# Kernel optimization log

Hardware: AMD Instinct MI355X
Metric: run time of the kernel (lower is better)

The kernel has to match this reference:

```python
import jax, jax.numpy as jnp
import numpy as np

T, B, OBS, D, H = 512, 256, 256, 512, 512  # time, batch, obs_dim, embed/gru hidden, critic hidden


def setup_inputs() -> dict:
    key = jax.random.key(0)
    ks = jax.random.split(key, 10)
    s = lambda fan_in: 1.0 / np.sqrt(fan_in)
    return {
        "obs": jax.random.normal(ks[0], (T, B, OBS), dtype=jnp.float32),
        "done": jax.random.bernoulli(ks[1], 0.01, (T, B)),
        "hstate": jnp.zeros((B, D), dtype=jnp.float32),
        # embedding dense
        "W_emb": jax.random.normal(ks[2], (OBS, D), dtype=jnp.float32) * s(OBS),
        "b_emb": jnp.zeros((D,), dtype=jnp.float32),
        # GRU: input kernels [D, 3D] (r|z|n), hidden kernels [D, 3D], input bias [3D], hn bias [D]
        "Wi": jax.random.normal(ks[3], (D, 3 * D), dtype=jnp.float32) * s(D),
        "bi": jnp.zeros((3 * D,), dtype=jnp.float32),
        "Wh": jax.random.normal(ks[4], (D, 3 * D), dtype=jnp.float32) * s(D),
        "bhn": jnp.zeros((D,), dtype=jnp.float32),
        # critic MLP
        "W1": jax.random.normal(ks[5], (D, H), dtype=jnp.float32) * s(D),
        "b1": jnp.zeros((H,), dtype=jnp.float32),
        "W2": jax.random.normal(ks[6], (H, 1), dtype=jnp.float32) * s(H),
        "b2": jnp.zeros((1,), dtype=jnp.float32),
    }


def _forward(obs, done, hstate, W_emb, b_emb, Wi, bi, Wh, bhn, W1, b1, W2, b2):
    # embedding: [T, B, D]
    emb = jax.nn.relu(jnp.einsum("tbo,od->tbd", obs, W_emb) + b_emb)
    # precompute input-side gate preactivations for all timesteps: [T, B, 3D]
    xg = jnp.einsum("tbd,de->tbe", emb, Wi) + bi

    def step(h, inp):
        xg_t, d_t = inp
        # reset carry where episode ended (flax GRU init carry is zeros)
        h = jnp.where(d_t[:, None], 0.0, h)
        hg = h @ Wh  # [B, 3D]
        r = jax.nn.sigmoid(xg_t[:, :D] + hg[:, :D])
        z = jax.nn.sigmoid(xg_t[:, D:2 * D] + hg[:, D:2 * D])
        n = jnp.tanh(xg_t[:, 2 * D:] + r * (hg[:, 2 * D:] + bhn))
        h_new = (1.0 - z) * n + z * h
        return h_new, h_new

    h_last, ys = jax.lax.scan(step, hstate, (xg, done))  # ys: [T, B, D]
    critic = jax.nn.relu(jnp.einsum("tbd,dh->tbh", ys, W1) + b1)
    value = jnp.squeeze(jnp.einsum("tbh,ho->tbo", critic, W2) + b2, axis=-1)  # [T, B]
    return h_last, value


def reference(obs, done, hstate, W_emb, b_emb, Wi, bi, Wh, bhn, W1, b1, W2, b2):
    return _forward(obs, done, hstate, W_emb, b_emb, Wi, bi, Wh, bhn, W1, b1, W2, b2)
```

## Files before the change

kernel.cpp:

```cpp
#include <hip/hip_runtime.h>

#define TT   512
#define BB   256
#define OBSD 256
#define DD   512
#define HH   512
#define MROWS (TT*BB)

typedef __attribute__((ext_vector_type(8))) short short8;
typedef __attribute__((ext_vector_type(4))) float f32x4;

__device__ __forceinline__ ushort f2b(float f){
  unsigned int x = __float_as_uint(f);
  x = (x + 0x7fffu + ((x >> 16) & 1u)) >> 16;
  return (ushort)x;
}
__device__ __forceinline__ float b2f(ushort u){
  return __uint_as_float(((unsigned int)u) << 16);
}
__device__ __forceinline__ float sigm(float x){ return 1.f/(1.f + __expf(-x)); }
__device__ __forceinline__ float tanh_f(float x){ return 1.f - 2.f/(__expf(2.f*x) + 1.f); }

__global__ void k_transpose_bf16(const float* __restrict__ W, ushort* __restrict__ Wt,
                                 int K, int N){
  int i = blockIdx.x*256 + threadIdx.x;
  if(i >= K*N) return;
  int k = i / N, n = i % N;
  Wt[(size_t)n*K + k] = f2b(W[i]);
}

__global__ void k_f32_to_bf16(const float* __restrict__ in, ushort* __restrict__ out,
                              int n4){
  int i = blockIdx.x*256 + threadIdx.x;
  if(i >= n4) return;
  const float4 v = ((const float4*)in)[i];
  union{ ushort u[4]; uint2 d; } p;
  p.u[0] = f2b(v.x); p.u[1] = f2b(v.y); p.u[2] = f2b(v.z); p.u[3] = f2b(v.w);
  ((uint2*)out)[i] = p.d;
}

__global__ void k_detect(const int* __restrict__ done, int* __restrict__ flag){
  __shared__ int cnt;
  if(threadIdx.x == 0) cnt = 0;
  __syncthreads();
  int c = 0;
  for(int i = threadIdx.x; i < 32768; i += 256) c += (done[i] != 0);
  for(int off = 32; off; off >>= 1) c += __shfl_down(c, off, 64);
  if((threadIdx.x & 63) == 0) atomicAdd(&cnt, c);
  __syncthreads();
  if(threadIdx.x == 0) *flag = (cnt > 700) ? 1 : 0;
}

#define GSTAGE(buf, k0v) { \
  _Pragma("unroll") \
  for(int j = 0; j < 2; j++){ \
    const int flat = tid*16 + j*4096;         \
    const int rw  = flat >> 6;                \
    const int ke  = (flat & 63) >> 1;         \
    __builtin_amdgcn_global_load_lds( \
      (const __attribute__((address_space(1))) void*)(A + (m0+rw)*(size_t)K + (k0v) + ke), \
      (__attribute__((address_space(3))) void*)((char*)As[buf] + flat), 16, 0, 0); \
    __builtin_amdgcn_global_load_lds( \
      (const __attribute__((address_space(1))) void*)(Bt + (n0+rw)*(size_t)K + (k0v) + ke), \
      (__attribute__((address_space(3))) void*)((char*)Bs[buf] + flat), 16, 0, 0); \
  } }
#define GCOMPUTE(buf) { \
    short8 af[4], bf[4]; \
    _Pragma("unroll") for(int mi=0;mi<4;mi++) \
      af[mi] = *(const short8*)((const char*)As[buf] + (wr*64+mi*16+l16)*64 + l4*16); \
    _Pragma("unroll") for(int ni=0;ni<4;ni++) \
      bf[ni] = *(const short8*)((const char*)Bs[buf] + (wc*64+ni*16+l16)*64 + l4*16); \
    _Pragma("unroll") for(int mi=0;mi<4;mi++) \
      _Pragma("unroll") for(int ni=0;ni<4;ni++) \
        acc[mi][ni] = __builtin_amdgcn_mfma_f32_16x16x32_bf16(af[mi], bf[ni], acc[mi][ni], 0,0,0); }

__global__ __launch_bounds__(256) void k_gemm128(const ushort* __restrict__ A,
                                                 const ushort* __restrict__ Bt,
                                                 const float* __restrict__ bias,
                                                 ushort* __restrict__ C,
                                                 int M, int N, int K, int relu,
                                                 int xg_layout,
                                                 float* __restrict__ vpart,
                                                 const float* __restrict__ W2f){
  __shared__ __align__(16) ushort As[2][4096];
  __shared__ __align__(16) ushort Bs[2][4096];
  const int tid = threadIdx.x;
  const int l = tid & 63, l16 = l & 15, l4 = l >> 4;
  const int w = tid >> 6, wr = w >> 1, wc = w & 1;
  const size_t m0 = (size_t)blockIdx.x*128, n0 = (size_t)blockIdx.y*128;
  f32x4 acc[4][4] = {};

  GSTAGE(0, 0);
  asm volatile("s_waitcnt vmcnt(0)" ::: "memory");
  __syncthreads();
  int cur = 0;
  for(int k0 = 32; k0 < K; k0 += 32){
    GSTAGE(cur^1, k0);
    GCOMPUTE(cur);
    asm volatile("s_waitcnt vmcnt(0)" ::: "memory");
    __syncthreads();
    cur ^= 1;
  }
  GCOMPUTE(cur);

  if(vpart){
    float w2v[4];
    float bv[4];
    #pragma unroll
    for(int ni=0;ni<4;ni++){
      const int col = (int)n0 + wc*64 + ni*16 + l16;
      w2v[ni] = W2f[col];
      bv[ni]  = bias[col];
    }
    #pragma unroll
    for(int mi=0;mi<4;mi++){
      #pragma unroll
      for(int r=0;r<4;r++){
        float s = 0.f;
        #pragma unroll
        for(int ni=0;ni<4;ni++){
          float v = acc[mi][ni][r] + bv[ni];
          v = fmaxf(v, 0.f);
          s += v * w2v[ni];
        }
        #pragma unroll
        for(int off=1; off<16; off<<=1) s += __shfl_xor(s, off, 16);
        if(l16 == 0){
          const int row = (int)m0 + wr*64 + mi*16 + l4*4 + r;
          vpart[(size_t)(blockIdx.y*2 + wc)*M + row] = s;
        }
      }
    }
    return;
  }

  #pragma unroll
  for(int ni=0;ni<4;ni++){
    const int col = (int)n0 + wc*64 + ni*16 + l16;
    const float bv = bias[col];
    #pragma unroll
    for(int mi=0;mi<4;mi++){
      #pragma unroll
      for(int r=0;r<4;r++){
        const int row = (int)m0 + wr*64 + mi*16 + l4*4 + r;
        float v = acc[mi][ni][r] + bv;
        if(relu) v = fmaxf(v, 0.f);
        size_t addr;
        if(xg_layout){
          const int tl = row >> 8, brow = row & 255;
          const int gg = brow >> 5, r32 = brow & 31;
          const int gate = col >> 9, cw = col & 511, ds2 = cw >> 4, c16 = cw & 15;
          addr = ((((size_t)tl*32 + ds2)*8 + gg)*3 + gate)*512 + r32*16 + c16;
        } else {
          addr = (size_t)row*N + col;
        }
        C[addr] = f2b(v);
      }
    }
  }
}

__global__ __launch_bounds__(256) void k_value_reduce(const float* __restrict__ vp,
                                                      const float* __restrict__ b2,
                                                      float* __restrict__ val, int M){
  int i = blockIdx.x*256 + threadIdx.x;
  if(i >= M) return;
  float s = b2[0];
  #pragma unroll
  for(int cb=0; cb<8; cb++) s += vp[(size_t)cb*M + i];
  val[i] = s;
}

__device__ __forceinline__ void bar_slow(int* cntA, int g, int ds, int target, int tid){
  asm volatile("s_waitcnt vmcnt(0)" ::: "memory");
  __syncthreads();
  if(tid == 0)
    __hip_atomic_store(cntA + g*32 + ds, target,
                       __ATOMIC_RELAXED, __HIP_MEMORY_SCOPE_AGENT);
  if(tid < 32){
    const int* fp = cntA + g*32 + tid;
    while(__hip_atomic_load(fp, __ATOMIC_RELAXED, __HIP_MEMORY_SCOPE_AGENT) < target)
      __builtin_amdgcn_s_sleep(1);
  }
  __syncthreads();
}

__device__ __forceinline__ void bar_fast(int* cntL, int* cntA, int g, int ds,
                                         int target, int tid){
  asm volatile("s_waitcnt vmcnt(0)" ::: "memory");
  __syncthreads();
  if(tid == 0){
    int* pL = cntL + g*32 + ds;
    asm volatile("global_atomic_swap %0, %1, off" :: "v"(pL), "v"(target) : "memory");
    __hip_atomic_store(cntA + g*32 + ds, target,
                       __ATOMIC_RELAXED, __HIP_MEMORY_SCOPE_AGENT);
  }
  if(tid < 32){
    int* fpL = cntL + g*32 + tid;
    const int* fpA = cntA + g*32 + tid;
    int it = 0;
    for(;;){
      int old;
      asm volatile("global_atomic_add %0, %1, %2, off sc0"
                   : "=v"(old) : "v"(fpL), "v"(0) : "memory");
      asm volatile("s_waitcnt vmcnt(0)" ::: "memory");
      if(old >= target) break;
      if((++it & 15) == 0 &&
         __hip_atomic_load(fpA, __ATOMIC_RELAXED, __HIP_MEMORY_SCOPE_AGENT) >= target)
        break;
      __builtin_amdgcn_s_sleep(1);
    }
  }
  __syncthreads();
  asm volatile("buffer_inv sc0" ::: "memory");
}

#define ALD_S(v, j) { const ushort* pj_ = hgrp + (j)*1024; \
  asm volatile("global_load_dwordx4 %0, %1, off sc0 sc1" : "=&v"(v) : "v"(pj_)); }
#define ALD_F(v, j) { const ushort* pj_ = hgrp + (j)*1024; \
  asm volatile("global_load_dwordx4 %0, %1, off" : "=&v"(v) : "v"(pj_)); }
#define DECL_A short8 a0,a1,a2,a3,a4,a5,a6,a7,a8,a9,a10,a11,a12,a13,a14,a15
#define ALOADS(M) M(a0,0);M(a1,1);M(a2,2);M(a3,3);M(a4,4);M(a5,5);M(a6,6);M(a7,7); \
  M(a8,8);M(a9,9);M(a10,10);M(a11,11);M(a12,12);M(a13,13);M(a14,14);M(a15,15)
#define ZERO_A { const short8 z = {0,0,0,0,0,0,0,0}; \
  a0=z;a1=z;a2=z;a3=z;a4=z;a5=z;a6=z;a7=z;a8=z;a9=z;a10=z;a11=z;a12=z;a13=z;a14=z;a15=z; }
#define STEPK(ak, k0lit) { const int kboff = ((k0lit + l4*8) << 1); \
  _Pragma("unroll") for(int gi=0; gi<3; gi++){ \
    const short8 wf = *(const short8*)((const char*)whs + ((rb[gi] + kboff) ^ sw[gi])); \
    acc[gi] = __builtin_amdgcn_mfma_f32_16x16x32_bf16(wf, ak, acc[gi], 0, 0, 0); } }
#define MFMA48 STEPK(a0,0) STEPK(a1,32) STEPK(a2,64) STEPK(a3,96) STEPK(a4,128) \
  STEPK(a5,160) STEPK(a6,192) STEPK(a7,224) STEPK(a8,256) STEPK(a9,288) STEPK(a10,320) \
  STEPK(a11,352) STEPK(a12,384) STEPK(a13,416) STEPK(a14,448) STEPK(a15,480)
#define XG_PREFETCH(tls, nb) { \
  const ushort* slb_ = xg + (((size_t)(tls)*32 + ds)*8 + g)*1536; \
  const int q0_ = m ? 512 : 0; \
  __builtin_amdgcn_global_load_lds( \
    (const __attribute__((address_space(1))) void*)(slb_ + q0_ + l*8), \
    (__attribute__((address_space(3))) void*)(&xgs[nb][q0_]), 16, 0, 0); \
  __builtin_amdgcn_global_load_lds( \
    (const __attribute__((address_space(1))) void*)(slb_ + 1024 + l*8), \
    (__attribute__((address_space(3))) void*)(&xgs[nb][1024]), 16, 0, 0); }
#define GRU_EPI(pv) { \
  const uint2 xru = *(const uint2*)&xgs[cur][        r32*16 + l4*4]; \
  const uint2 xzu = *(const uint2*)&xgs[cur][ 512 +  r32*16 + l4*4]; \
  const uint2 xnu = *(const uint2*)&xgs[cur][1024 +  r32*16 + l4*4]; \
  const ushort xr4[4] = {(ushort)(xru.x&0xffff),(ushort)(xru.x>>16), \
                         (ushort)(xru.y&0xffff),(ushort)(xru.y>>16)}; \
  const ushort xz4[4] = {(ushort)(xzu.x&0xffff),(ushort)(xzu.x>>16), \
                         (ushort)(xzu.y&0xffff),(ushort)(xzu.y>>16)}; \
  const ushort xn4[4] = {(ushort)(xnu.x&0xffff),(ushort)(xnu.x>>16), \
                         (ushort)(xnu.y&0xffff),(ushort)(xnu.y>>16)}; \
  const float bhv[4] = {bh4.x, bh4.y, bh4.z, bh4.w}; \
  union{ ushort u[4]; uint2 v; } p; \
  _Pragma("unroll") for(int r=0;r<4;r++){ \
    const float hold = dn ? 0.f : hf[r]; \
    const float rg = sigm(b2f(xr4[r]) + acc[0][r]); \
    const float zg = sigm(b2f(xz4[r]) + acc[1][r]); \
    const float ng = tanh_f(b2f(xn4[r]) + rg*(acc[2][r] + bhv[r])); \
    const float hv = (1.f - zg)*ng + zg*hold; \
    hf[r] = hv; p.u[r] = f2b(hv); } \
  pv = p.v; }

__global__ __launch_bounds__(128, 1) void k_scan_coop(
    const ushort* __restrict__ xg,
    const void* __restrict__ donep,
    const int* __restrict__ flagp, const float* __restrict__ h_in,
    const ushort* __restrict__ WhT, const float* __restrict__ bhn,
    ushort* __restrict__ ys, float* __restrict__ h_io,
    float* __restrict__ h_last, ushort* __restrict__ hbf,
    int t0, int steps, int* __restrict__ cntbase, int* __restrict__ xcc_tab){
  __shared__ __align__(16) ushort whs[48*512];
  __shared__ __align__(16) ushort xgs[2][1536];
  __shared__ unsigned char dns[512*32];
  __shared__ int fastf;
  const int tid = threadIdx.x;
  const int m = tid >> 6, l = tid & 63, l16 = l & 15, l4 = l >> 4;
  const int bid = blockIdx.x;
  const int g = bid & 7, ds = bid >> 3;
  const int use8 = *flagp;
  const unsigned char* d8 = (const unsigned char*)donep;
  const int* d32 = (const int*)donep;
  int* cntL = cntbase;
  int* cntA = cntbase + 256;

  for(int e = tid; e < 3072; e += 128){
    const int lr = e >> 6;
    const int kc = (e & 63) << 3;
    const int grow_w = (lr >> 4)*DD + ds*16 + (lr & 15);
    short8 v = *(const short8*)(WhT + (size_t)grow_w*DD + kc);
    int boff = ((lr << 10) + (kc << 1)) ^ ((lr & 7) << 4);
    *(short8*)((char*)whs + boff) = v;
  }
  for(int e = tid; e < steps*32; e += 128){
    const int tloc = e >> 5, r = e & 31;
    const int gi = (t0 + tloc)*BB + g*32 + r;
    dns[e] = use8 ? (d8[gi] != 0) : (d32[gi] != 0);
  }

  const int r32 = m*16 + l16;
  const int row = g*32 + r32;
  const int d0  = ds*16 + l4*4;
  const float4 bh4 = *(const float4*)(bhn + d0);

  float hf[4];
  {
    const float4 hv4 = *(const float4*)(h_in + (size_t)row*DD + d0);
    hf[0]=hv4.x; hf[1]=hv4.y; hf[2]=hv4.z; hf[3]=hv4.w;
    union{ ushort u[4]; uint2 v; } p;
    #pragma unroll
    for(int r=0;r<4;r++) p.u[r] = f2b(hf[r]);
    const ushort* pp = hbf + (size_t)g*16384 + ds*512 + r32*16 + l4*4;
    asm volatile("global_store_dwordx2 %0, %1, off sc0 sc1" :: "v"(pp), "v"(p.v) : "memory");
  }
  XG_PREFETCH(0, 0);
  int my_xcc;
  asm volatile("s_getreg_b32 %0, hwreg(HW_REG_XCC_ID)" : "=s"(my_xcc));
  if(tid == 0){
    int* p = xcc_tab + bid;
    asm volatile("global_store_dword %0, %1, off sc0 sc1" :: "v"(p), "v"(my_xcc) : "memory");
  }
  bar_slow(cntA, g, ds, 1, tid);
  {
    int bad = 0;
    if(tid < 32){
      const int* p = xcc_tab + tid*8 + g;
      int v;
      asm volatile("global_load_dword %0, %1, off sc0 sc1" : "=v"(v) : "v"(p) : "memory");
      asm volatile("s_waitcnt vmcnt(0)" ::: "memory");
      bad = (v != my_xcc);
    }
    const int anybad = __any(bad);
    if(tid == 0) fastf = !anybad;
    __syncthreads();
  }
  const int fast = fastf;

  int rb[3], sw[3];
  #pragma unroll
  for(int gi=0; gi<3; gi++){
    const int lr = gi*16 + l16;
    rb[gi] = lr << 10;
    sw[gi] = (lr & 7) << 4;
  }
  const ushort* hb0 = hbf;
  const ushort* hb1 = hbf + (size_t)BB*DD;
  const size_t csub = (size_t)((l4>>1) << 9) + (size_t)r32*16 + ((l4&1) << 3);
  int cur = 0;

  if(fast){
    asm volatile("buffer_inv sc0" ::: "memory");
    for(int tl = 0; tl < steps; tl++){
      const ushort* hcur = (tl & 1) ? hb1 : hb0;
      ushort* hnxt = (ushort*)((tl & 1) ? hb0 : hb1);
      const bool dn = dns[tl*32 + r32];
      const ushort* hgrp = hcur + (size_t)g*16384 + csub;
      DECL_A;
      ALOADS(ALD_F);
      __builtin_amdgcn_sched_barrier(0);
      if(tl + 1 < steps){
        XG_PREFETCH(tl+1, cur^1);
        __builtin_amdgcn_sched_barrier(0);
        asm volatile("s_waitcnt vmcnt(2)" ::: "memory");
      } else {
        asm volatile("s_waitcnt vmcnt(0)" ::: "memory");
      }
      __builtin_amdgcn_sched_barrier(0);
      if(__builtin_expect(dn, 0)) ZERO_A;
      f32x4 acc[3] = {};
      MFMA48;
      uint2 pv;
      GRU_EPI(pv);
      const ushort* pp = hnxt + (size_t)g*16384 + ds*512 + r32*16 + l4*4;
      asm volatile("global_store_dwordx2 %0, %1, off" :: "v"(pp), "v"(pv) : "memory");
      bar_fast(cntL, cntA, g, ds, tl + 2, tid);
      *(uint2*)(ys + ((size_t)tl*BB + row)*DD + d0) = pv;
      cur ^= 1;
    }
  } else {
    for(int tl = 0; tl < steps; tl++){
      const ushort* hcur = (tl & 1) ? hb1 : hb0;
      ushort* hnxt = (ushort*)((tl & 1) ? hb0 : hb1);
      const bool dn = dns[tl*32 + r32];
      const ushort* hgrp = hcur + (size_t)g*16384 + csub;
      DECL_A;
      ALOADS(ALD_S);
      __builtin_amdgcn_sched_barrier(0);
      if(tl + 1 < steps){
        XG_PREFETCH(tl+1, cur^1);
        __builtin_amdgcn_sched_barrier(0);
        asm volatile("s_waitcnt vmcnt(2)" ::: "memory");
      } else {
        asm volatile("s_waitcnt vmcnt(0)" ::: "memory");
      }
      __builtin_amdgcn_sched_barrier(0);
      if(__builtin_expect(dn, 0)) ZERO_A;
      f32x4 acc[3] = {};
      MFMA48;
      uint2 pv;
      GRU_EPI(pv);
      const ushort* pp = hnxt + (size_t)g*16384 + ds*512 + r32*16 + l4*4;
      asm volatile("global_store_dwordx2 %0, %1, off sc0 sc1" :: "v"(pp), "v"(pv) : "memory");
      bar_slow(cntA, g, ds, tl + 2, tid);
      *(uint2*)(ys + ((size_t)tl*BB + row)*DD + d0) = pv;
      cur ^= 1;
    }
  }

  {
    float4 o; o.x=hf[0]; o.y=hf[1]; o.z=hf[2]; o.w=hf[3];
    *(float4*)(h_io   + (size_t)row*DD + d0) = o;
    *(float4*)(h_last + (size_t)row*DD + d0) = o;
  }
}

__global__ __launch_bounds__(1024) void k_scan(const ushort* __restrict__ xg,
                                               const void* __restrict__ donep,
                                               const int* __restrict__ flagp,
                                               const float* __restrict__ h_in,
                                               const ushort* __restrict__ WhT,
                                               const float* __restrict__ bhn,
                                               ushort* __restrict__ ys,
                                               float* __restrict__ h_io,
                                               float* __restrict__ h_last,
                                               int t0, int steps){
  __shared__ __align__(16) float  h_f[16][DD];
  __shared__ __align__(16) ushort h_b[16][DD];
  const int tid = threadIdx.x;
  const int w = tid >> 6, l = tid & 63, l16 = l & 15, l4 = l >> 4;
  const int b0 = blockIdx.x * 16;
  const int use8 = *flagp;
  const unsigned char* d8 = (const unsigned char*)donep;
  const int* d32 = (const int*)donep;

  for(int e = tid; e < 16*DD; e += 1024){
    int b = e >> 9, dd = e & (DD-1);
    float v = h_in[(size_t)(b0 + b)*DD + dd];
    h_f[b][dd] = v; h_b[b][dd] = f2b(v);
  }
  __syncthreads();

  const int dbase = w * 32;
  const ushort* bp[6];
  #pragma unroll
  for(int g=0; g<3; g++)
    #pragma unroll
    for(int nt=0; nt<2; nt++)
      bp[g*2+nt] = WhT + (size_t)(g*DD + dbase + nt*16 + l16) * DD;

  for(int tl = 0; tl < steps; tl++){
    const int drow = (t0 + tl)*BB + b0;
    const bool dnA = use8 ? (d8[drow + l16] != 0) : (d32[drow + l16] != 0);
    f32x4 acc[3][2] = {};
    const short8 zf = {0,0,0,0,0,0,0,0};
    for(int k0 = 0; k0 < DD; k0 += 32){
      const int kb = k0 + l4*8;
      short8 a = *(const short8*)&h_b[l16][kb];
      if(dnA) a = zf;
      #pragma unroll
      for(int g=0; g<3; g++)
        #pragma unroll
        for(int nt=0; nt<2; nt++){
          const short8 b = *(const short8*)(bp[g*2+nt] + kb);
          acc[g][nt] = __builtin_amdgcn_mfma_f32_16x16x32_bf16(a, b, acc[g][nt], 0, 0, 0);
        }
    }
    float hnew[2][4];
    #pragma unroll
    for(int nt=0; nt<2; nt++){
      const int dd = dbase + nt*16 + l16;
      const float bh = bhn[dd];
      const int ds2 = dd >> 4, c16 = dd & 15;
      #pragma unroll
      for(int r=0; r<4; r++){
        const int brow = l4*4 + r;
        const int grow = b0 + brow;
        const int gg = grow >> 5, r32 = grow & 31;
        const bool dn = use8 ? (d8[drow + brow] != 0) : (d32[drow + brow] != 0);
        const size_t sbase = (((size_t)tl*32 + ds2)*8 + gg)*1536 + r32*16 + c16;
        const float xr = b2f(xg[sbase]);
        const float xz = b2f(xg[sbase + 512]);
        const float xn = b2f(xg[sbase + 1024]);
        const float hold = dn ? 0.f : h_f[brow][dd];
        const float rg = sigm(xr + acc[0][nt][r]);
        const float zg = sigm(xz + acc[1][nt][r]);
        const float ng = tanh_f(xn + rg*(acc[2][nt][r] + bh));
        hnew[nt][r] = (1.f - zg)*ng + zg*hold;
      }
    }
    __syncthreads();
    #pragma unroll
    for(int nt=0; nt<2; nt++){
      const int dd = dbase + nt*16 + l16;
      #pragma unroll
      for(int r=0; r<4; r++){
        const int brow = l4*4 + r;
        const size_t rowl = (size_t)(tl*BB + b0 + brow);
        const float hv = hnew[nt][r];
        h_f[brow][dd] = hv;
        h_b[brow][dd] = f2b(hv);
        ys[rowl*DD + dd] = f2b(hv);
      }
    }
    __syncthreads();
  }

  for(int e = tid; e < 16*DD; e += 1024){
    int b = e >> 9, dd = e & (DD-1);
    float v = h_f[b][dd];
    h_io[(size_t)(b0 + b)*DD + dd] = v;
    h_last[(size_t)(b0 + b)*DD + dd] = v;
  }
}

extern "C" void kernel_launch(void* const* d_in, const int* in_sizes, int n_in,
                              void* d_out, int out_size, void* d_ws, size_t ws_size,
                              hipStream_t stream){
  const float* obs    = (const float*)d_in[0];
  const void*  done   = d_in[1];
  const float* hstate = (const float*)d_in[2];
  const float* W_emb  = (const float*)d_in[3];
  const float* b_emb  = (const float*)d_in[4];
  const float* Wi     = (const float*)d_in[5];
  const float* bi     = (const float*)d_in[6];
  const float* Wh     = (const float*)d_in[7];
  const float* bhn    = (const float*)d_in[8];
  const float* W1     = (const float*)d_in[9];
  const float* b1     = (const float*)d_in[10];
  const float* W2     = (const float*)d_in[11];
  const float* b2     = (const float*)d_in[12];
  float* out = (float*)d_out;
  char*  ws  = (char*)d_ws;

  ushort* WembT = (ushort*)(ws + 0);
  ushort* WiT   = (ushort*)(ws + 262144);
  ushort* WhT   = (ushort*)(ws + 1835008);
  ushort* W1T   = (ushort*)(ws + 3407872);
  int*    flag  = (int*)   (ws + 3932160);
  float*  hio   = (float*) (ws + 3936256);
  ushort* hbf   = (ushort*)(ws + 4460544);
  int*    cnt   = (int*)   (ws + 4984832);
  int*    xcc   = (int*)   (ws + 5017600);
  const size_t FIX = 5242880;

  int TC = 0;
  {
    const int cands[6] = {512, 256, 128, 64, 32, 16};
    for(int i = 0; i < 6; i++){
      size_t need = FIX + (size_t)cands[i] * 1310720u;
      if(need <= ws_size){ TC = cands[i]; break; }
    }
  }
  if(TC == 0) return;

  ushort* emb_c  = (ushort*)(ws + FIX);
  ushort* xg_c   = (ushort*)(ws + FIX + (size_t)TC*262144u);
  ushort* ys_c   = (ushort*)(ws + FIX + (size_t)TC*1048576u);
  float*  vpart  = (float*)emb_c;
  ushort* obs_bf = ys_c;

  k_transpose_bf16<<<(OBSD*DD+255)/256, 256, 0, stream>>>(W_emb, WembT, OBSD, DD);
  k_transpose_bf16<<<(DD*3*DD+255)/256, 256, 0, stream>>>(Wi, WiT, DD, 3*DD);
  k_transpose_bf16<<<(DD*3*DD+255)/256, 256, 0, stream>>>(Wh, WhT, DD, 3*DD);
  k_transpose_bf16<<<(DD*HH+255)/256, 256, 0, stream>>>(W1, W1T, DD, HH);
  k_detect<<<1, 256, 0, stream>>>((const int*)done, flag);

  const int nchunks = TT / TC;
  for(int c = 0; c < nchunks; c++){
    const int Mc = TC * BB;
    const size_t row0 = (size_t)c * Mc;
    k_f32_to_bf16<<<(Mc*OBSD/4 + 255)/256, 256, 0, stream>>>(obs + row0*OBSD, obs_bf,
                                                             Mc*OBSD/4);
    k_gemm128<<<dim3(Mc/128, DD/128), 256, 0, stream>>>(obs_bf, WembT, b_emb,
                                                        emb_c, Mc, DD, OBSD, 1, 0,
                                                        nullptr, nullptr);
    k_gemm128<<<dim3(Mc/128, (3*DD)/128), 256, 0, stream>>>(emb_c, WiT, bi,
                                                            xg_c, Mc, 3*DD, DD, 0, 1,
                                                            nullptr, nullptr);
    {
      const ushort* xg_a = xg_c;  const void* done_a = done;
      const int* flag_a = flag;   const float* hin_a = (c == 0) ? hstate : hio;
      const ushort* wht_a = WhT;  const float* bhn_a = bhn;
      ushort* ys_a = ys_c;        float* hio_a = hio;
      float* hl_a = out;          ushort* hbf_a = hbf;
      int t0_a = c*TC;            int steps_a = TC;
      int* cnt_a = cnt;           int* xcc_a = xcc;
      void* args[14] = { (void*)&xg_a, (void*)&done_a, (void*)&flag_a, (void*)&hin_a,
                         (void*)&wht_a, (void*)&bhn_a, (void*)&ys_a, (void*)&hio_a,
                         (void*)&hl_a, (void*)&hbf_a, (void*)&t0_a, (void*)&steps_a,
                         (void*)&cnt_a, (void*)&xcc_a };
      hipMemsetAsync(cnt, 0, 4096, stream);
      hipError_t err = hipLaunchCooperativeKernel((const void*)k_scan_coop,
                                                  dim3(256), dim3(128), args, 0, stream);
      if(err != hipSuccess){
        k_scan<<<16, 1024, 0, stream>>>(xg_c, done, flag, hin_a, WhT, bhn,
                                        ys_c, hio, out, c*TC, TC);
      }
    }
    k_gemm128<<<dim3(Mc/128, HH/128), 256, 0, stream>>>(ys_c, W1T, b1,
                                                        nullptr, Mc, HH, DD, 1, 0,
                                                        vpart, W2);
    k_value_reduce<<<(Mc + 255)/256, 256, 0, stream>>>(vpart, b2,
                                                       out + (size_t)BB*DD + row0, Mc);
  }
}
```

Baseline: 2.783 ms.

## Fuse critic MLP into cooperative GRU scan using per-step hidden loads

The critic first layer and its W2 reduction now run inside the scan kernel. Each block keeps a 16-column slice of W1 in shared memory and reuses the hidden-state fragments it already loads for step t to compute the critic output for step t-1. Per-block partial values go to a 32-way partial buffer, which a reduce kernel sums. This drops the ys write and the separate critic GEMM pass, but adds 16 MFMAs plus shuffles to every serial scan step and another 16 KB of LDS. The non-cooperative fallback keeps the old path.

```diff
diff --git a/kernel.cpp b/kernel.cpp
--- a/kernel.cpp
+++ b/kernel.cpp
@@ -104,8 +104,7 @@
   GCOMPUTE(cur);
 
   if(vpart){
-    float w2v[4];
-    float bv[4];
+    float w2v[4], bv[4];
     #pragma unroll
     for(int ni=0;ni<4;ni++){
       const int col = (int)n0 + wc*64 + ni*16 + l16;
@@ -162,12 +161,12 @@
 
 __global__ __launch_bounds__(256) void k_value_reduce(const float* __restrict__ vp,
                                                       const float* __restrict__ b2,
-                                                      float* __restrict__ val, int M){
+                                                      float* __restrict__ val, int M,
+                                                      int nparts){
   int i = blockIdx.x*256 + threadIdx.x;
   if(i >= M) return;
   float s = b2[0];
-  #pragma unroll
-  for(int cb=0; cb<8; cb++) s += vp[(size_t)cb*M + i];
+  for(int cb = 0; cb < nparts; cb++) s += vp[(size_t)cb*M + i];
   val[i] = s;
 }
 
@@ -231,6 +230,21 @@
 #define MFMA48 STEPK(a0,0) STEPK(a1,32) STEPK(a2,64) STEPK(a3,96) STEPK(a4,128) \
   STEPK(a5,160) STEPK(a6,192) STEPK(a7,224) STEPK(a8,256) STEPK(a9,288) STEPK(a10,320) \
   STEPK(a11,352) STEPK(a12,384) STEPK(a13,416) STEPK(a14,448) STEPK(a15,480)
+#define CSTEP(ak, k0lit) { const int kboff = ((k0lit + l4*8) << 1); \
+  const short8 wf = *(const short8*)((const char*)w1s + ((rbc + kboff) ^ swc)); \
+  accc = __builtin_amdgcn_mfma_f32_16x16x32_bf16(wf, ak, accc, 0, 0, 0); }
+#define CRITIC16 CSTEP(a0,0) CSTEP(a1,32) CSTEP(a2,64) CSTEP(a3,96) CSTEP(a4,128) \
+  CSTEP(a5,160) CSTEP(a6,192) CSTEP(a7,224) CSTEP(a8,256) CSTEP(a9,288) CSTEP(a10,320) \
+  CSTEP(a11,352) CSTEP(a12,384) CSTEP(a13,416) CSTEP(a14,448) CSTEP(a15,480)
+#define CRITIC_EPI(tcr) { \
+  float s = 0.f; \
+  _Pragma("unroll") for(int r=0;r<4;r++){ \
+    float v = accc[r] + b1v[r]; \
+    v = fmaxf(v, 0.f); \
+    s += v * w2v[r]; } \
+  s += __shfl_xor(s, 16, 64); \
+  s += __shfl_xor(s, 32, 64); \
+  if(l4 == 0) vpart[(size_t)ds*Mc + (size_t)(tcr)*BB + row] = s; }
 #define XG_PREFETCH(tls, nb) { \
   const ushort* slb_ = xg + (((size_t)(tls)*32 + ds)*8 + g)*1536; \
   const int q0_ = m ? 512 : 0; \
@@ -265,11 +279,15 @@
     const ushort* __restrict__ xg,
     const void* __restrict__ donep,
     const int* __restrict__ flagp, const float* __restrict__ h_in,
-    const ushort* __restrict__ WhT, const float* __restrict__ bhn,
-    ushort* __restrict__ ys, float* __restrict__ h_io,
-    float* __restrict__ h_last, ushort* __restrict__ hbf,
+    const ushort* __restrict__ WhT, const ushort* __restrict__ W1T,
+    const float* __restrict__ bhn, const float* __restrict__ b1,
+    const float* __restrict__ W2f,
+    float* __restrict__ h_io, float* __restrict__ h_last,
+    ushort* __restrict__ hbf,
+    float* __restrict__ vpart,
     int t0, int steps, int* __restrict__ cntbase, int* __restrict__ xcc_tab){
   __shared__ __align__(16) ushort whs[48*512];
+  __shared__ __align__(16) ushort w1s[16*512];
   __shared__ __align__(16) ushort xgs[2][1536];
   __shared__ unsigned char dns[512*32];
   __shared__ int fastf;
@@ -282,6 +300,7 @@
   const int* d32 = (const int*)donep;
   int* cntL = cntbase;
   int* cntA = cntbase + 256;
+  const int Mc = steps*BB;
 
   for(int e = tid; e < 3072; e += 128){
     const int lr = e >> 6;
@@ -291,6 +310,13 @@
     int boff = ((lr << 10) + (kc << 1)) ^ ((lr & 7) << 4);
     *(short8*)((char*)whs + boff) = v;
   }
+  for(int e = tid; e < 1024; e += 128){
+    const int lr = e >> 6;
+    const int kc = (e & 63) << 3;
+    short8 v = *(const short8*)(W1T + (size_t)(ds*16 + lr)*DD + kc);
+    int boff = ((lr << 10) + (kc << 1)) ^ ((lr & 7) << 4);
+    *(short8*)((char*)w1s + boff) = v;
+  }
   for(int e = tid; e < steps*32; e += 128){
     const int tloc = e >> 5, r = e & 31;
     const int gi = (t0 + tloc)*BB + g*32 + r;
@@ -301,6 +327,14 @@
   const int row = g*32 + r32;
   const int d0  = ds*16 + l4*4;
   const float4 bh4 = *(const float4*)(bhn + d0);
+  float b1v[4], w2v[4];
+  {
+    const float4 b1f = *(const float4*)(b1 + d0);
+    const float4 w2f = *(const float4*)(W2f + d0);
+    b1v[0]=b1f.x; b1v[1]=b1f.y; b1v[2]=b1f.z; b1v[3]=b1f.w;
+    w2v[0]=w2f.x; w2v[1]=w2f.y; w2v[2]=w2f.z; w2v[3]=w2f.w;
+  }
+  const int rbc = l16 << 10, swc = (l16 & 7) << 4;
 
   float hf[4];
   {
@@ -365,6 +399,11 @@
         asm volatile("s_waitcnt vmcnt(0)" ::: "memory");
       }
       __builtin_amdgcn_sched_barrier(0);
+      f32x4 accc = {};
+      if(tl > 0){
+        CRITIC16;
+        CRITIC_EPI(tl-1);
+      }
       if(__builtin_expect(dn, 0)) ZERO_A;
       f32x4 acc[3] = {};
       MFMA48;
@@ -373,8 +412,18 @@
       const ushort* pp = hnxt + (size_t)g*16384 + ds*512 + r32*16 + l4*4;
       asm volatile("global_store_dwordx2 %0, %1, off" :: "v"(pp), "v"(pv) : "memory");
       bar_fast(cntL, cntA, g, ds, tl + 2, tid);
-      *(uint2*)(ys + ((size_t)tl*BB + row)*DD + d0) = pv;
       cur ^= 1;
+    }
+    {
+      const ushort* hfin = (steps & 1) ? hb1 : hb0;
+      const ushort* hgrp = hfin + (size_t)g*16384 + csub;
+      DECL_A;
+      ALOADS(ALD_F);
+      asm volatile("s_waitcnt vmcnt(0)" ::: "memory");
+      __builtin_amdgcn_sched_barrier(0);
+      f32x4 accc = {};
+      CRITIC16;
+      CRITIC_EPI(steps-1);
     }
   } else {
     for(int tl = 0; tl < steps; tl++){
@@ -393,6 +442,11 @@
         asm volatile("s_waitcnt vmcnt(0)" ::: "memory");
       }
       __builtin_amdgcn_sched_barrier(0);
+      f32x4 accc = {};
+      if(tl > 0){
+        CRITIC16;
+        CRITIC_EPI(tl-1);
+      }
       if(__builtin_expect(dn, 0)) ZERO_A;
       f32x4 acc[3] = {};
       MFMA48;
@@ -401,8 +455,18 @@
       const ushort* pp = hnxt + (size_t)g*16384 + ds*512 + r32*16 + l4*4;
       asm volatile("global_store_dwordx2 %0, %1, off sc0 sc1" :: "v"(pp), "v"(pv) : "memory");
       bar_slow(cntA, g, ds, tl + 2, tid);
-      *(uint2*)(ys + ((size_t)tl*BB + row)*DD + d0) = pv;
       cur ^= 1;
+    }
+    {
+      const ushort* hfin = (steps & 1) ? hb1 : hb0;
+      const ushort* hgrp = hfin + (size_t)g*16384 + csub;
+      DECL_A;
+      ALOADS(ALD_S);
+      asm volatile("s_waitcnt vmcnt(0)" ::: "memory");
+      __builtin_amdgcn_sched_barrier(0);
+      f32x4 accc = {};
+      CRITIC16;
+      CRITIC_EPI(steps-1);
     }
   }
 
@@ -576,30 +640,40 @@
     k_gemm128<<<dim3(Mc/128, (3*DD)/128), 256, 0, stream>>>(emb_c, WiT, bi,
                                                             xg_c, Mc, 3*DD, DD, 0, 1,
                                                             nullptr, nullptr);
+    hipError_t err;
     {
       const ushort* xg_a = xg_c;  const void* done_a = done;
       const int* flag_a = flag;   const float* hin_a = (c == 0) ? hstate : hio;
-      const ushort* wht_a = WhT;  const float* bhn_a = bhn;
-      ushort* ys_a = ys_c;        float* hio_a = hio;
-      float* hl_a = out;          ushort* hbf_a = hbf;
+      const ushort* wht_a = WhT;  const ushort* w1t_a = W1T;
+      const float* bhn_a = bhn;   const float* b1_a = b1;
+      const float* w2_a = W2;
+      float* hio_a = hio;         float* hl_a = out;
+      ushort* hbf_a = hbf;        float* vp_a = vpart;
       int t0_a = c*TC;            int steps_a = TC;
       int* cnt_a = cnt;           int* xcc_a = xcc;
-      void* args[14] = { (void*)&xg_a, (void*)&done_a, (void*)&flag_a, (void*)&hin_a,
-                         (void*)&wht_a, (void*)&bhn_a, (void*)&ys_a, (void*)&hio_a,
-                         (void*)&hl_a, (void*)&hbf_a, (void*)&t0_a, (void*)&steps_a,
+      void* args[17] = { (void*)&xg_a, (void*)&done_a, (void*)&flag_a, (void*)&hin_a,
+                         (void*)&wht_a, (void*)&w1t_a, (void*)&bhn_a, (void*)&b1_a,
+                         (void*)&w2_a, (void*)&hio_a, (void*)&hl_a, (void*)&hbf_a,
+                         (void*)&vp_a, (void*)&t0_a, (void*)&steps_a,
                          (void*)&cnt_a, (void*)&xcc_a };
       hipMemsetAsync(cnt, 0, 4096, stream);
-      hipError_t err = hipLaunchCooperativeKernel((const void*)k_scan_coop,
-                                                  dim3(256), dim3(128), args, 0, stream);
-      if(err != hipSuccess){
-        k_scan<<<16, 1024, 0, stream>>>(xg_c, done, flag, hin_a, WhT, bhn,
-                                        ys_c, hio, out, c*TC, TC);
-      }
-    }
-    k_gemm128<<<dim3(Mc/128, HH/128), 256, 0, stream>>>(ys_c, W1T, b1,
-                                                        nullptr, Mc, HH, DD, 1, 0,
-                                                        vpart, W2);
-    k_value_reduce<<<(Mc + 255)/256, 256, 0, stream>>>(vpart, b2,
-                                                       out + (size_t)BB*DD + row0, Mc);
-  }
-}
+      err = hipLaunchCooperativeKernel((const void*)k_scan_coop,
+                                       dim3(256), dim3(128), args, 0, stream);
+    }
+    if(err == hipSuccess){
+      k_value_reduce<<<(Mc + 255)/256, 256, 0, stream>>>(vpart, b2,
+                                                         out + (size_t)BB*DD + row0,
+                                                         Mc, 32);
+    } else {
+      const float* hin_a = (c == 0) ? hstate : hio;
+      k_scan<<<16, 1024, 0, stream>>>(xg_c, done, flag, hin_a, WhT, bhn,
+                                      ys_c, hio, out, c*TC, TC);
+      k_gemm128<<<dim3(Mc/128, HH/128), 256, 0, stream>>>(ys_c, W1T, b1,
+                                                          nullptr, Mc, HH, DD, 1, 0,
+                                                          vpart, W2);
+      k_value_reduce<<<(Mc + 255)/256, 256, 0, stream>>>(vpart, b2,
+                                                         out + (size_t)BB*DD + row0,
+                                                         Mc, 8);
+    }
+  }
+}
```

After: 2.883 ms. 3.6% more time.

## Split GRU scan into 512 single-wave blocks over 16-row batch groups

Applied to the files above, without the earlier changes.

The cooperative GRU scan moves from 256 blocks of two waves (32 batch rows per group) to 512 blocks of one wave (16 rows per group). The xg layout, hidden-state buffer layout, done-flag staging, barrier counter offsets and xcc table indexing are all rewritten for 16-row groups. The aim is to shrink intra-block synchronisation and spread the recurrence across more independent blocks. The cost is that each block still stages the full Wh slice into LDS, so weight-loading traffic and LDS use per CU double, and more blocks take part in the cross-block barriers.

```diff
diff --git a/kernel.cpp b/kernel.cpp
--- a/kernel.cpp
+++ b/kernel.cpp
@@ -104,8 +104,7 @@
   GCOMPUTE(cur);
 
   if(vpart){
-    float w2v[4];
-    float bv[4];
+    float w2v[4], bv[4];
     #pragma unroll
     for(int ni=0;ni<4;ni++){
       const int col = (int)n0 + wc*64 + ni*16 + l16;
@@ -148,9 +147,9 @@
         size_t addr;
         if(xg_layout){
           const int tl = row >> 8, brow = row & 255;
-          const int gg = brow >> 5, r32 = brow & 31;
+          const int gg = brow >> 4, r16 = brow & 15;
           const int gate = col >> 9, cw = col & 511, ds2 = cw >> 4, c16 = cw & 15;
-          addr = ((((size_t)tl*32 + ds2)*8 + gg)*3 + gate)*512 + r32*16 + c16;
+          addr = ((((size_t)tl*32 + ds2)*16 + gg)*3 + gate)*256 + r16*16 + c16;
         } else {
           addr = (size_t)row*N + col;
         }
@@ -162,12 +161,12 @@
 
 __global__ __launch_bounds__(256) void k_value_reduce(const float* __restrict__ vp,
                                                       const float* __restrict__ b2,
-                                                      float* __restrict__ val, int M){
+                                                      float* __restrict__ val, int M,
+                                                      int nparts){
   int i = blockIdx.x*256 + threadIdx.x;
   if(i >= M) return;
   float s = b2[0];
-  #pragma unroll
-  for(int cb=0; cb<8; cb++) s += vp[(size_t)cb*M + i];
+  for(int cb = 0; cb < nparts; cb++) s += vp[(size_t)cb*M + i];
   val[i] = s;
 }
 
@@ -215,9 +214,9 @@
   asm volatile("buffer_inv sc0" ::: "memory");
 }
 
-#define ALD_S(v, j) { const ushort* pj_ = hgrp + (j)*1024; \
+#define ALD_S(v, j) { const ushort* pj_ = hgrp + (j)*512; \
   asm volatile("global_load_dwordx4 %0, %1, off sc0 sc1" : "=&v"(v) : "v"(pj_)); }
-#define ALD_F(v, j) { const ushort* pj_ = hgrp + (j)*1024; \
+#define ALD_F(v, j) { const ushort* pj_ = hgrp + (j)*512; \
   asm volatile("global_load_dwordx4 %0, %1, off" : "=&v"(v) : "v"(pj_)); }
 #define DECL_A short8 a0,a1,a2,a3,a4,a5,a6,a7,a8,a9,a10,a11,a12,a13,a14,a15
 #define ALOADS(M) M(a0,0);M(a1,1);M(a2,2);M(a3,3);M(a4,4);M(a5,5);M(a6,6);M(a7,7); \
@@ -232,18 +231,18 @@
   STEPK(a5,160) STEPK(a6,192) STEPK(a7,224) STEPK(a8,256) STEPK(a9,288) STEPK(a10,320) \
   STEPK(a11,352) STEPK(a12,384) STEPK(a13,416) STEPK(a14,448) STEPK(a15,480)
 #define XG_PREFETCH(tls, nb) { \
-  const ushort* slb_ = xg + (((size_t)(tls)*32 + ds)*8 + g)*1536; \
-  const int q0_ = m ? 512 : 0; \
+  const ushort* slb_ = xg + (((size_t)(tls)*32 + ds)*16 + g)*768; \
   __builtin_amdgcn_global_load_lds( \
-    (const __attribute__((address_space(1))) void*)(slb_ + q0_ + l*8), \
-    (__attribute__((address_space(3))) void*)(&xgs[nb][q0_]), 16, 0, 0); \
+    (const __attribute__((address_space(1))) void*)(slb_ + l*8), \
+    (__attribute__((address_space(3))) void*)(&xgs[nb][0]), 16, 0, 0); \
   __builtin_amdgcn_global_load_lds( \
-    (const __attribute__((address_space(1))) void*)(slb_ + 1024 + l*8), \
-    (__attribute__((address_space(3))) void*)(&xgs[nb][1024]), 16, 0, 0); }
+    (const __attribute__((address_space(1))) void*)(slb_ + 256 + l*8), \
+    (__attribute__((address_space(3))) void*)(&xgs[nb][256]), 16, 0, 0); }
 #define GRU_EPI(pv) { \
-  const uint2 xru = *(const uint2*)&xgs[cur][        r32*16 + l4*4]; \
-  const uint2 xzu = *(const uint2*)&xgs[cur][ 512 +  r32*16 + l4*4]; \
-  const uint2 xnu = *(const uint2*)&xgs[cur][1024 +  r32*16 + l4*4]; \
+  const int xb = l16*16 + l4*4; \
+  const uint2 xru = *(const uint2*)&xgs[cur][      xb]; \
+  const uint2 xzu = *(const uint2*)&xgs[cur][256 + xb]; \
+  const uint2 xnu = *(const uint2*)&xgs[cur][512 + xb]; \
   const ushort xr4[4] = {(ushort)(xru.x&0xffff),(ushort)(xru.x>>16), \
                          (ushort)(xru.y&0xffff),(ushort)(xru.y>>16)}; \
   const ushort xz4[4] = {(ushort)(xzu.x&0xffff),(ushort)(xzu.x>>16), \
@@ -261,7 +260,7 @@
     hf[r] = hv; p.u[r] = f2b(hv); } \
   pv = p.v; }
 
-__global__ __launch_bounds__(128, 1) void k_scan_coop(
+__global__ __launch_bounds__(64, 1) void k_scan_coop(
     const ushort* __restrict__ xg,
     const void* __restrict__ donep,
     const int* __restrict__ flagp, const float* __restrict__ h_in,
@@ -270,20 +269,21 @@
     float* __restrict__ h_last, ushort* __restrict__ hbf,
     int t0, int steps, int* __restrict__ cntbase, int* __restrict__ xcc_tab){
   __shared__ __align__(16) ushort whs[48*512];
-  __shared__ __align__(16) ushort xgs[2][1536];
-  __shared__ unsigned char dns[512*32];
+  __shared__ __align__(16) ushort xgs[2][768];
+  __shared__ unsigned char dns[512*16];
   __shared__ int fastf;
   const int tid = threadIdx.x;
-  const int m = tid >> 6, l = tid & 63, l16 = l & 15, l4 = l >> 4;
+  const int l = tid, l16 = l & 15, l4 = l >> 4;
   const int bid = blockIdx.x;
-  const int g = bid & 7, ds = bid >> 3;
+  const int g = ((bid & 7) << 1) | ((bid >> 3) & 1);
+  const int ds = bid >> 4;
   const int use8 = *flagp;
   const unsigned char* d8 = (const unsigned char*)donep;
   const int* d32 = (const int*)donep;
   int* cntL = cntbase;
-  int* cntA = cntbase + 256;
-
-  for(int e = tid; e < 3072; e += 128){
+  int* cntA = cntbase + 512;
+
+  for(int e = tid; e < 3072; e += 64){
     const int lr = e >> 6;
     const int kc = (e & 63) << 3;
     const int grow_w = (lr >> 4)*DD + ds*16 + (lr & 15);
@@ -291,14 +291,13 @@
     int boff = ((lr << 10) + (kc << 1)) ^ ((lr & 7) << 4);
     *(short8*)((char*)whs + boff) = v;
   }
-  for(int e = tid; e < steps*32; e += 128){
-    const int tloc = e >> 5, r = e & 31;
-    const int gi = (t0 + tloc)*BB + g*32 + r;
+  for(int e = tid; e < steps*16; e += 64){
+    const int tloc = e >> 4, r = e & 15;
+    const int gi = (t0 + tloc)*BB + g*16 + r;
     dns[e] = use8 ? (d8[gi] != 0) : (d32[gi] != 0);
   }
 
-  const int r32 = m*16 + l16;
-  const int row = g*32 + r32;
+  const int row = g*16 + l16;
   const int d0  = ds*16 + l4*4;
   const float4 bh4 = *(const float4*)(bhn + d0);
 
@@ -309,7 +308,7 @@
     union{ ushort u[4]; uint2 v; } p;
     #pragma unroll
     for(int r=0;r<4;r++) p.u[r] = f2b(hf[r]);
-    const ushort* pp = hbf + (size_t)g*16384 + ds*512 + r32*16 + l4*4;
+    const ushort* pp = hbf + (size_t)g*8192 + ds*256 + l16*16 + l4*4;
     asm volatile("global_store_dwordx2 %0, %1, off sc0 sc1" :: "v"(pp), "v"(p.v) : "memory");
   }
   XG_PREFETCH(0, 0);
@@ -323,7 +322,7 @@
   {
     int bad = 0;
     if(tid < 32){
-      const int* p = xcc_tab + tid*8 + g;
+      const int* p = xcc_tab + tid*16 + (g & 1)*8 + (g >> 1);
       int v;
       asm volatile("global_load_dword %0, %1, off sc0 sc1" : "=v"(v) : "v"(p) : "memory");
       asm volatile("s_waitcnt vmcnt(0)" ::: "memory");
@@ -344,7 +343,7 @@
   }
   const ushort* hb0 = hbf;
   const ushort* hb1 = hbf + (size_t)BB*DD;
-  const size_t csub = (size_t)((l4>>1) << 9) + (size_t)r32*16 + ((l4&1) << 3);
+  const size_t csub = (size_t)((l4>>1) << 8) + (size_t)l16*16 + ((l4&1) << 3);
   int cur = 0;
 
   if(fast){
@@ -352,8 +351,8 @@
     for(int tl = 0; tl < steps; tl++){
       const ushort* hcur = (tl & 1) ? hb1 : hb0;
       ushort* hnxt = (ushort*)((tl & 1) ? hb0 : hb1);
-      const bool dn = dns[tl*32 + r32];
-      const ushort* hgrp = hcur + (size_t)g*16384 + csub;
+      const bool dn = dns[tl*16 + l16];
+      const ushort* hgrp = hcur + (size_t)g*8192 + csub;
       DECL_A;
       ALOADS(ALD_F);
       __builtin_amdgcn_sched_barrier(0);
@@ -370,7 +369,7 @@
       MFMA48;
       uint2 pv;
       GRU_EPI(pv);
-      const ushort* pp = hnxt + (size_t)g*16384 + ds*512 + r32*16 + l4*4;
+      const ushort* pp = hnxt + (size_t)g*8192 + ds*256 + l16*16 + l4*4;
       asm volatile("global_store_dwordx2 %0, %1, off" :: "v"(pp), "v"(pv) : "memory");
       bar_fast(cntL, cntA, g, ds, tl + 2, tid);
       *(uint2*)(ys + ((size_t)tl*BB + row)*DD + d0) = pv;
@@ -380,8 +379,8 @@
     for(int tl = 0; tl < steps; tl++){
       const ushort* hcur = (tl & 1) ? hb1 : hb0;
       ushort* hnxt = (ushort*)((tl & 1) ? hb0 : hb1);
-      const bool dn = dns[tl*32 + r32];
-      const ushort* hgrp = hcur + (size_t)g*16384 + csub;
+      const bool dn = dns[tl*16 + l16];
+      const ushort* hgrp = hcur + (size_t)g*8192 + csub;
       DECL_A;
       ALOADS(ALD_S);
       __builtin_amdgcn_sched_barrier(0);
@@ -398,7 +397,7 @@
       MFMA48;
       uint2 pv;
       GRU_EPI(pv);
-      const ushort* pp = hnxt + (size_t)g*16384 + ds*512 + r32*16 + l4*4;
+      const ushort* pp = hnxt + (size_t)g*8192 + ds*256 + l16*16 + l4*4;
       asm volatile("global_store_dwordx2 %0, %1, off sc0 sc1" :: "v"(pp), "v"(pv) : "memory");
       bar_slow(cntA, g, ds, tl + 2, tid);
       *(uint2*)(ys + ((size_t)tl*BB + row)*DD + d0) = pv;
@@ -474,12 +473,12 @@
       for(int r=0; r<4; r++){
         const int brow = l4*4 + r;
         const int grow = b0 + brow;
-        const int gg = grow >> 5, r32 = grow & 31;
+        const int gg = grow >> 4, r16 = grow & 15;
         const bool dn = use8 ? (d8[drow + brow] != 0) : (d32[drow + brow] != 0);
-        const size_t sbase = (((size_t)tl*32 + ds2)*8 + gg)*1536 + r32*16 + c16;
+        const size_t sbase = ((((size_t)tl*32 + ds2)*16 + gg)*3)*256 + r16*16 + c16;
         const float xr = b2f(xg[sbase]);
-        const float xz = b2f(xg[sbase + 512]);
-        const float xn = b2f(xg[sbase + 1024]);
+        const float xz = b2f(xg[sbase + 256]);
+        const float xn = b2f(xg[sbase + 512]);
         const float hold = dn ? 0.f : h_f[brow][dd];
         const float rg = sigm(xr + acc[0][nt][r]);
         const float zg = sigm(xz + acc[1][nt][r]);
@@ -590,7 +589,7 @@
                          (void*)&cnt_a, (void*)&xcc_a };
       hipMemsetAsync(cnt, 0, 4096, stream);
       hipError_t err = hipLaunchCooperativeKernel((const void*)k_scan_coop,
-                                                  dim3(256), dim3(128), args, 0, stream);
+                                                  dim3(512), dim3(64), args, 0, stream);
       if(err != hipSuccess){
         k_scan<<<16, 1024, 0, stream>>>(xg_c, done, flag, hin_a, WhT, bhn,
                                         ys_c, hio, out, c*TC, TC);
@@ -600,6 +599,6 @@
                                                         nullptr, Mc, HH, DD, 1, 0,
                                                         vpart, W2);
     k_value_reduce<<<(Mc + 255)/256, 256, 0, stream>>>(vpart, b2,
-                                                       out + (size_t)BB*DD + row0, Mc);
-  }
-}
+                                                       out + (size_t)BB*DD + row0, Mc, 8);
+  }
+}
```

Result: slower. 3.204 ms (+15.1%).
